# Kernel tuning notes

Hardware: AMD Instinct MI355X
Metric: run time of the kernel (lower is better)

Reference implementation:

```python
import jax, jax.numpy as jnp
import numpy as np

MARGIN = 0.0625  # init kwarg `margin`; barrier = relu


def setup_inputs() -> dict:
    key = jax.random.key(0)
    k1, k2, k3, k4 = jax.random.split(key, 4)
    B, N, M = 64, 64, 100000
    return {
        "outputs": jax.random.normal(k1, (B, N, 3), dtype=jnp.float32),
        "c2ws": jax.random.normal(k2, (B, 4, 4), dtype=jnp.float32),
        "scene_scales": jax.random.uniform(k3, (B,), dtype=jnp.float32),
        "means": jax.random.normal(k4, (M, 3), dtype=jnp.float32),
    }


def reference(outputs, c2ws, scene_scales, means):
    # aff = R * s (per-batch scaled rotation block), trans = translation column
    aff = c2ws[:, :3, :3] * scene_scales[:, None, None]      # [B,3,3]
    trans = c2ws[:, :3, 3]                                   # [B,3]
    # retrajs = baddbmm(trans, outputs, aff.mT) = outputs @ aff^T + trans
    retrajs = jnp.einsum("bnj,bij->bni", outputs, aff) + trans[:, None, :]
    q = retrajs.reshape(-1, 3)                               # [Q,3], Q = B*N
    # Brute-force nearest neighbor (replaces kd_tree.query); torch_kdtree
    # returns SQUARED euclidean distances, so we keep d^2.
    # d2[q,m] = |q|^2 + |m|^2 - 2 q.m  -> [Q,M] (the dominant memory-bound op)
    d2 = (
        jnp.sum(q * q, axis=-1, keepdims=True)
        + jnp.sum(means * means, axis=-1)[None, :]
        - 2.0 * (q @ means.T)
    )
    dists = jnp.maximum(jnp.min(d2, axis=1), 0.0)            # [Q]
    loss = jnp.mean(jax.nn.relu(-(dists - MARGIN)))
    return loss
```

## Files before the change

kernel.cpp:

```cpp
#include <hip/hip_runtime.h>

#define MARGIN 0.0625f

#define P 4096
#define M 100000

#define NC 36
#define NCELLS (NC * NC * NC)
#define GMIN (-4.5f)
#define INVC 4.0f

#define CAP 256

typedef float float4v __attribute__((ext_vector_type(4)));

#define WS_CNT_OFF    0
#define WS_BUCKET_OFF 186880

static __device__ __forceinline__ int cell1(float v) {
    int c = (int)floorf((v - GMIN) * INVC);
    return min(max(c, 0), NC - 1);
}

__global__ __launch_bounds__(256) void scatter_kernel(
    const float* __restrict__ means,
    unsigned int* __restrict__ cnt,
    float4v* __restrict__ bucket,
    float* __restrict__ out)
{
    int idx = blockIdx.x * 256 + threadIdx.x;
    if (idx == 0) out[0] = 0.0f;
    if (idx < M) {
        const float* mp = means + 3 * idx;
        float x = mp[0], y = mp[1], z = mp[2];
        int c = (cell1(z) * NC + cell1(y)) * NC + cell1(x);
        unsigned int slot = atomicAdd(&cnt[c], 1u);
        if (slot < CAP)
            bucket[(size_t)c * CAP + slot] =
                (float4v){-2.0f * x, -2.0f * y, -2.0f * z,
                          fmaf(x, x, fmaf(y, y, z * z))};
    }
}

__global__ __launch_bounds__(256, 4) void query_kernel(
    const float* __restrict__ outputs,
    const float* __restrict__ c2ws,
    const float* __restrict__ scales,
    const unsigned int* __restrict__ cnt,
    const float4v* __restrict__ bucket,
    float* __restrict__ out)
{
    const int t    = threadIdx.x;
    const int lane = t & 63;
    const int bid = (int)blockIdx.x;
    const int qb  = (bid & 7) * 128 + (bid >> 3);
    const int qi  = qb * 4 + (t >> 6);

    const int b = qi >> 6;
    const float s  = scales[b];
    const float o0 = outputs[3 * qi + 0];
    const float o1 = outputs[3 * qi + 1];
    const float o2 = outputs[3 * qi + 2];
    const float* cw = c2ws + b * 16;
    float q0 = fmaf(s, fmaf(cw[0],  o0, fmaf(cw[1],  o1, cw[2]  * o2)), cw[3]);
    float q1 = fmaf(s, fmaf(cw[4],  o0, fmaf(cw[5],  o1, cw[6]  * o2)), cw[7]);
    float q2 = fmaf(s, fmaf(cw[8],  o0, fmaf(cw[9],  o1, cw[10] * o2)), cw[11]);
    float qq = fmaf(q0, q0, fmaf(q1, q1, q2 * q2));

    const int cx = cell1(q0), cy = cell1(q1), cz = cell1(q2);

    int c27[27];
#pragma unroll
    for (int j = 0; j < 27; ++j) {
        int zz = min(max(cz + (j / 9) - 1,     0), NC - 1);
        int yy = min(max(cy + ((j / 3) % 3) - 1, 0), NC - 1);
        int xx = min(max(cx + (j % 3) - 1,     0), NC - 1);
        c27[j] = (zz * NC + yy) * NC + xx;
    }
    int n27[27];
#pragma unroll
    for (int j = 0; j < 27; ++j)
        n27[j] = min((int)cnt[c27[j]], CAP);

    int tot = 0;
#pragma unroll
    for (int j = 0; j < 27; ++j) tot += n27[j];

    float mn = 1e30f;
    if (tot > 0) {
#pragma unroll
        for (int j = 0; j < 27; ++j) {
            const int n = n27[j];
            if (n == 0) continue;
            const float4v* row = bucket + (size_t)c27[j] * CAP;
            {
                float4v mv = row[min(lane, n - 1)];
                float d = fmaf(q2, mv[2], fmaf(q1, mv[1],
                          fmaf(q0, mv[0], mv[3])));
                mn = fminf(mn, d);
            }
            if (n > 64) {
                float4v mv = row[min(64 + lane, n - 1)];
                float d = fmaf(q2, mv[2], fmaf(q1, mv[1],
                          fmaf(q0, mv[0], mv[3])));
                mn = fminf(mn, d);
            }
            if (n > 128) {
                for (int k = 128 + lane; k < n; k += 64) {
                    float4v mv = row[k];
                    float d = fmaf(q2, mv[2], fmaf(q1, mv[1],
                              fmaf(q0, mv[0], mv[3])));
                    mn = fminf(mn, d);
                }
            }
        }
#pragma unroll
        for (int off = 32; off > 0; off >>= 1)
            mn = fminf(mn, __shfl_xor(mn, off, 64));
    }

    float v = 0.0f;
    if (lane == 0) {
        float d = fmaxf(qq + mn, 0.0f);
        v = fmaxf(MARGIN - d, 0.0f) * (1.0f / (float)P);
    }

    __shared__ float red[4];
    if (lane == 0) red[t >> 6] = v;
    __syncthreads();
    if (t == 0)
        atomicAdd(out, red[0] + red[1] + red[2] + red[3]);
}

extern "C" void kernel_launch(void* const* d_in, const int* in_sizes, int n_in,
                              void* d_out, int out_size, void* d_ws, size_t ws_size,
                              hipStream_t stream) {
    const float* outputs = (const float*)d_in[0];
    const float* c2ws    = (const float*)d_in[1];
    const float* scales  = (const float*)d_in[2];
    const float* means   = (const float*)d_in[3];

    char* ws = (char*)d_ws;
    unsigned int* cnt    = (unsigned int*)(ws + WS_CNT_OFF);
    float4v*      bucket = (float4v*)(ws + WS_BUCKET_OFF);
    float*        out    = (float*)d_out;

    hipMemsetAsync(cnt, 0, NCELLS * sizeof(unsigned int), stream);
    scatter_kernel<<<(M + 255) / 256, 256, 0, stream>>>(means, cnt, bucket, out);
    query_kernel<<<P / 4, 256, 0, stream>>>(outputs, c2ws, scales,
                                            cnt, bucket, out);
}
```

Measured before the change: 93.58 us.

## Prune neighbor cells by margin lower bound and use one-wave blocks

Each query now computes the per-axis squared distance from the query to each of the 27 neighbor cells and skips any cell whose lower bound already reaches the margin, since such points cannot contribute to the relu loss. Blocks shrink to one wavefront per query with a direct atomicAdd, which removes the shared-memory reduction and the barrier. Cell scanning is also restructured per z-slab so only nine counts are held live at once. The pruning relies on the loss ignoring distances at or above the margin, and the extra atomics and smaller blocks may add contention or scheduling overhead.

```diff
diff --git a/kernel.cpp b/kernel.cpp
--- a/kernel.cpp
+++ b/kernel.cpp
@@ -8,6 +8,7 @@
 #define NC 36
 #define NCELLS (NC * NC * NC)
 #define GMIN (-4.5f)
+#define CW 0.25f
 #define INVC 4.0f
 
 #define CAP 256
@@ -42,7 +43,13 @@
     }
 }
 
-__global__ __launch_bounds__(256, 4) void query_kernel(
+static __device__ __forceinline__ float axdist(float q, int kk) {
+    float lo = (kk == 0)      ? -1e30f : GMIN + kk * CW;
+    float hi = (kk == NC - 1) ?  1e30f : GMIN + (kk + 1) * CW;
+    return fmaxf(fmaxf(lo - q, q - hi), 0.0f);
+}
+
+__global__ __launch_bounds__(64, 8) void query_kernel(
     const float* __restrict__ outputs,
     const float* __restrict__ c2ws,
     const float* __restrict__ scales,
@@ -50,11 +57,9 @@
     const float4v* __restrict__ bucket,
     float* __restrict__ out)
 {
-    const int t    = threadIdx.x;
-    const int lane = t & 63;
+    const int lane = threadIdx.x;
     const int bid = (int)blockIdx.x;
-    const int qb  = (bid & 7) * 128 + (bid >> 3);
-    const int qi  = qb * 4 + (t >> 6);
+    const int qi  = (bid & 7) * 512 + (bid >> 3);
 
     const int b = qi >> 6;
     const float s  = scales[b];
@@ -69,67 +74,63 @@
 
     const int cx = cell1(q0), cy = cell1(q1), cz = cell1(q2);
 
-    int c27[27];
+    int   kx[3], ky[3], kz[3];
+    float dx2[3], dy2[3], dz2[3];
 #pragma unroll
-    for (int j = 0; j < 27; ++j) {
-        int zz = min(max(cz + (j / 9) - 1,     0), NC - 1);
-        int yy = min(max(cy + ((j / 3) % 3) - 1, 0), NC - 1);
-        int xx = min(max(cx + (j % 3) - 1,     0), NC - 1);
-        c27[j] = (zz * NC + yy) * NC + xx;
+    for (int o = 0; o < 3; ++o) {
+        kx[o] = min(max(cx + o - 1, 0), NC - 1);
+        ky[o] = min(max(cy + o - 1, 0), NC - 1);
+        kz[o] = min(max(cz + o - 1, 0), NC - 1);
+        float ax = axdist(q0, kx[o]); dx2[o] = ax * ax;
+        float ay = axdist(q1, ky[o]); dy2[o] = ay * ay;
+        float az = axdist(q2, kz[o]); dz2[o] = az * az;
     }
-    int n27[27];
-#pragma unroll
-    for (int j = 0; j < 27; ++j)
-        n27[j] = min((int)cnt[c27[j]], CAP);
-
-    int tot = 0;
-#pragma unroll
-    for (int j = 0; j < 27; ++j) tot += n27[j];
 
     float mn = 1e30f;
-    if (tot > 0) {
 #pragma unroll
-        for (int j = 0; j < 27; ++j) {
-            const int n = n27[j];
+    for (int iz = 0; iz < 3; ++iz) {
+        int n9[9], c9[9];
+#pragma unroll
+        for (int j = 0; j < 9; ++j) {
+            const int iy = j / 3, ix = j % 3;
+            const float lb = dz2[iz] + dy2[iy] + dx2[ix];
+            c9[j] = (kz[iz] * NC + ky[iy]) * NC + kx[ix];
+            n9[j] = (lb < MARGIN) ? min((int)cnt[c9[j]], CAP) : 0;
+        }
+#pragma unroll
+        for (int j = 0; j < 9; ++j) {
+            const int n = n9[j];
             if (n == 0) continue;
-            const float4v* row = bucket + (size_t)c27[j] * CAP;
+            const float4v* row = bucket + (size_t)c9[j] * CAP;
             {
                 float4v mv = row[min(lane, n - 1)];
-                float d = fmaf(q2, mv[2], fmaf(q1, mv[1],
-                          fmaf(q0, mv[0], mv[3])));
-                mn = fminf(mn, d);
+                mn = fminf(mn, fmaf(q2, mv[2], fmaf(q1, mv[1],
+                               fmaf(q0, mv[0], mv[3]))));
             }
             if (n > 64) {
                 float4v mv = row[min(64 + lane, n - 1)];
-                float d = fmaf(q2, mv[2], fmaf(q1, mv[1],
-                          fmaf(q0, mv[0], mv[3])));
-                mn = fminf(mn, d);
+                mn = fminf(mn, fmaf(q2, mv[2], fmaf(q1, mv[1],
+                               fmaf(q0, mv[0], mv[3]))));
             }
             if (n > 128) {
                 for (int k = 128 + lane; k < n; k += 64) {
                     float4v mv = row[k];
-                    float d = fmaf(q2, mv[2], fmaf(q1, mv[1],
-                              fmaf(q0, mv[0], mv[3])));
-                    mn = fminf(mn, d);
+                    mn = fminf(mn, fmaf(q2, mv[2], fmaf(q1, mv[1],
+                                   fmaf(q0, mv[0], mv[3]))));
                 }
             }
         }
-#pragma unroll
-        for (int off = 32; off > 0; off >>= 1)
-            mn = fminf(mn, __shfl_xor(mn, off, 64));
     }
 
-    float v = 0.0f;
+#pragma unroll
+    for (int off = 32; off > 0; off >>= 1)
+        mn = fminf(mn, __shfl_xor(mn, off, 64));
+
     if (lane == 0) {
         float d = fmaxf(qq + mn, 0.0f);
-        v = fmaxf(MARGIN - d, 0.0f) * (1.0f / (float)P);
+        float v = fmaxf(MARGIN - d, 0.0f) * (1.0f / (float)P);
+        atomicAdd(out, v);
     }
-
-    __shared__ float red[4];
-    if (lane == 0) red[t >> 6] = v;
-    __syncthreads();
-    if (t == 0)
-        atomicAdd(out, red[0] + red[1] + red[2] + red[3]);
 }
 
 extern "C" void kernel_launch(void* const* d_in, const int* in_sizes, int n_in,
@@ -147,6 +148,6 @@
 
     hipMemsetAsync(cnt, 0, NCELLS * sizeof(unsigned int), stream);
     scatter_kernel<<<(M + 255) / 256, 256, 0, stream>>>(means, cnt, bucket, out);
-    query_kernel<<<P / 4, 256, 0, stream>>>(outputs, c2ws, scales,
-                                            cnt, bucket, out);
+    query_kernel<<<P, 64, 0, stream>>>(outputs, c2ws, scales,
+                                       cnt, bucket, out);
 }
```

New measurement: 128.8 us. 37.7% more time.
